# Performance work log

Hardware: AMD Instinct MI355X
Metric: run time of the kernel (lower is better)

The kernel has to match this reference:

```python
import jax, jax.numpy as jnp
import numpy as np

C = 128          # channels
N = 100000       # cells per rank (rank 0,1,2)
E_A0, E_A1, E_I1, E_I2 = 400000, 400000, 200000, 300000
NI = {"a0": 3, "a1": 6, "i1": 3, "i2": 6}   # invariant feature dims per relation
FACTOR = {"u0": 2, "u1": 3, "u2": 2}          # update-MLP concat factors


def setup_inputs() -> dict:
    key = jax.random.key(0)
    ks = iter(jax.random.split(key, 64))
    d = {}
    for name in ("f0", "f1", "f2"):
        d[name] = jax.random.normal(next(ks), (N, C), dtype=jnp.float32)
    for name, E in (("a0", E_A0), ("a1", E_A1), ("i1", E_I1), ("i2", E_I2)):
        d[name + "_send"] = jax.random.randint(next(ks), (E,), 0, N)
        d[name + "_recv"] = jax.random.randint(next(ks), (E,), 0, N)
        d["inv_" + name] = jax.random.uniform(next(ks), (E, NI[name]), dtype=jnp.float32)
        fin = 2 * C + NI[name]
        d[name + "_W1"] = jax.random.normal(next(ks), (fin, C), dtype=jnp.float32) / np.sqrt(fin)
        d[name + "_b1"] = jnp.zeros((C,), jnp.float32)
        d[name + "_W2"] = jax.random.normal(next(ks), (C, C), dtype=jnp.float32) / np.sqrt(C)
        d[name + "_b2"] = jnp.zeros((C,), jnp.float32)
        d[name + "_Wg"] = jax.random.normal(next(ks), (C, 1), dtype=jnp.float32) / np.sqrt(C)
        d[name + "_bg"] = jnp.zeros((1,), jnp.float32)
    for name, f in FACTOR.items():
        d[name + "_W1"] = jax.random.normal(next(ks), (f * C, C), dtype=jnp.float32) / np.sqrt(f * C)
        d[name + "_b1"] = jnp.zeros((C,), jnp.float32)
        d[name + "_W2"] = jax.random.normal(next(ks), (C, C), dtype=jnp.float32) / np.sqrt(C)
        d[name + "_b2"] = jnp.zeros((C,), jnp.float32)
    return d


def _econv(x_src, x_tgt, send, recv, inv, W1, b1, W2, b2, Wg, bg):
    # EConv: gather endpoints, per-edge 2-layer MLP on [x_s, x_t, invariants],
    # gated by a sigmoid edge-inference scalar (with_weighted_message=True).
    m = jnp.concatenate([x_src[send], x_tgt[recv], inv], axis=1)  # (E, 2C+ninv)
    m = jax.nn.silu(m @ W1 + b1)                                   # (E, C)
    m = jax.nn.silu(m @ W2 + b2)                                   # (E, C)
    gate = jax.nn.sigmoid(m @ Wg + bg)                             # (E, 1)
    return m * gate


def _aggregate(msg, recv, n):
    # ScatterAggregation: scatter-sum to target cells, then silu update.
    return jax.nn.silu(jax.ops.segment_sum(msg, recv, num_segments=n))


def _update(h, W1, b1, W2, b2):
    # update MLP: Linear -> SiLU -> Linear
    return jax.nn.silu(h @ W1 + b1) @ W2 + b2


def reference(f0, f1, f2,
              a0_send, a0_recv, inv_a0, a0_W1, a0_b1, a0_W2, a0_b2, a0_Wg, a0_bg,
              a1_send, a1_recv, inv_a1, a1_W1, a1_b1, a1_W2, a1_b2, a1_Wg, a1_bg,
              i1_send, i1_recv, inv_i1, i1_W1, i1_b1, i1_W2, i1_b2, i1_Wg, i1_bg,
              i2_send, i2_recv, inv_i2, i2_W1, i2_b1, i2_W2, i2_b2, i2_Wg, i2_bg,
              u0_W1, u0_b1, u0_W2, u0_b2,
              u1_W1, u1_b1, u1_W2, u1_b2,
              u2_W1, u2_b1, u2_W2, u2_b2):
    # same-rank messages (rank 0 and 1 adjacency)
    m_a0 = _aggregate(_econv(f0, f0, a0_send, a0_recv, inv_a0, a0_W1, a0_b1, a0_W2, a0_b2, a0_Wg, a0_bg), a0_recv, N)
    m_a1 = _aggregate(_econv(f1, f1, a1_send, a1_recv, inv_a1, a1_W1, a1_b1, a1_W2, a1_b2, a1_Wg, a1_bg), a1_recv, N)
    # low-to-high messages (incidence rank 0->1 and 1->2)
    m_i1 = _aggregate(_econv(f0, f1, i1_send, i1_recv, inv_i1, i1_W1, i1_b1, i1_W2, i1_b2, i1_Wg, i1_bg), i1_recv, N)
    m_i2 = _aggregate(_econv(f1, f2, i2_send, i2_recv, inv_i2, i2_W1, i2_b1, i2_W2, i2_b2, i2_Wg, i2_bg), i2_recv, N)
    # concat features with aggregated messages, update, residual add
    h0 = _update(jnp.concatenate([f0, m_a0], axis=1), u0_W1, u0_b1, u0_W2, u0_b2)
    h1 = _update(jnp.concatenate([f1, m_a1, m_i1], axis=1), u1_W1, u1_b1, u1_W2, u1_b2)
    h2 = _update(jnp.concatenate([f2, m_i2], axis=1), u2_W1, u2_b1, u2_W2, u2_b2)
    return jnp.stack([f0 + h0, f1 + h1, f2 + h2])  # (3, N, C)
```

## Files before the change

### kernel.cpp

```cpp
#include <hip/hip_runtime.h>
#include <hip/hip_bf16.h>
#include <cstdint>
#include <cstddef>

#define CDIM 128
#define NCELLS 100000

typedef __attribute__((ext_vector_type(8))) short short8;
typedef __attribute__((ext_vector_type(4))) float f32x4;

__device__ __forceinline__ unsigned short f2bf(float f) {
    unsigned u = __float_as_uint(f);
    unsigned r = u + 0x7FFFu + ((u >> 16) & 1u);
    return (unsigned short)(r >> 16);
}
__device__ __forceinline__ float bf2f(unsigned short u) {
    return __uint_as_float(((unsigned)u) << 16);
}
__device__ __forceinline__ float lo16(unsigned u) { return __uint_as_float(u << 16); }
__device__ __forceinline__ float hi16(unsigned u) { return __uint_as_float(u & 0xffff0000u); }
__device__ __forceinline__ unsigned pkbf(float lo, float hi) {
    unsigned r;
    asm("v_cvt_pk_bf16_f32 %0, %1, %2" : "=v"(r) : "v"(lo), "v"(hi));
    return r;
}
__device__ __forceinline__ unsigned short cvt1bf(float x) {
    return (unsigned short)(pkbf(x, x) & 0xffffu);
}
__device__ __forceinline__ float sigf(float x) {
    return __builtin_amdgcn_rcpf(1.f + __expf(-x));
}
__device__ __forceinline__ float siluf(float x) { return x * sigf(x); }

__device__ __forceinline__ unsigned silu2(unsigned a, unsigned b) {
    float lo = lo16(a) + lo16(b);
    float hi = hi16(a) + hi16(b);
    return pkbf(siluf(lo), siluf(hi));
}
__device__ __forceinline__ unsigned silu1(unsigned a) {
    return pkbf(siluf(lo16(a)), siluf(hi16(a)));
}

__device__ __forceinline__ void atomic_pk_bf16(void* addr, unsigned data) {
    asm volatile("global_atomic_pk_add_bf16 %0, %1, off"
                 :: "v"((unsigned long long)(uintptr_t)addr), "v"(data) : "memory");
}

__device__ __forceinline__ void load_lds16(const void* g, void* ldsbase, int lane) {
    __builtin_amdgcn_global_load_lds(
        (const __attribute__((address_space(1))) unsigned int*)(uintptr_t)g,
        (__attribute__((address_space(3))) unsigned int*)(uintptr_t)ldsbase,
        16, 0, 0);
}

struct PrepArgs {
    const float* src[14];
    int dstoff[14];
    int fin[14];
    int ktc[14];
    int tend[14];
};

__global__ void prep_kernel(PrepArgs pa, unsigned short* __restrict__ wb) {
    int tile = blockIdx.x;
    int m = 0;
    while (tile >= pa.tend[m]) m++;
    int local = tile - (m == 0 ? 0 : pa.tend[m - 1]);
    int ktc = pa.ktc[m];
    int ct = local / ktc;
    int kt = local % ktc;
    int l = threadIdx.x;
    unsigned short* dst = wb + pa.dstoff[m] + (size_t)local * 512 + l * 8;
    const float* src = pa.src[m];
    int fin = pa.fin[m];
    int col = ct * 16 + (l & 15);
#pragma unroll
    for (int i = 0; i < 8; i++) {
        int k = kt * 32 + (l >> 4) * 8 + i;
        float v = (k < fin) ? src[(size_t)k * CDIM + col] : 0.f;
        dst[i] = f2bf(v);
    }
}

__global__ void hist4_kernel(const int* __restrict__ r0, const int* __restrict__ r1,
                             const int* __restrict__ r2, const int* __restrict__ r3,
                             int E0, int E1, int E2, int E3, int* __restrict__ bins) {
    int i = blockIdx.x * blockDim.x + threadIdx.x;
    const int c1 = E0, c2 = c1 + E1, c3 = c2 + E2, c4 = c3 + E3;
    if (i >= c4) return;
    const int* r; int* b; int j;
    if (i < c1)      { r = r0; j = i;      b = bins; }
    else if (i < c2) { r = r1; j = i - c1; b = bins + (size_t)NCELLS; }
    else if (i < c3) { r = r2; j = i - c2; b = bins + (size_t)2 * NCELLS; }
    else             { r = r3; j = i - c3; b = bins + (size_t)3 * NCELLS; }
    atomicAdd(&b[r[j]], 1);
}

__global__ __launch_bounds__(1024)
void scan_kernel(const int* __restrict__ bins, int* __restrict__ offs, int NB) {
    __shared__ int wsum[16];
    __shared__ int run_s;
    const int r = blockIdx.x, t = threadIdx.x;
    const int lane = t & 63, w = t >> 6;
    const int* b = bins + (size_t)r * NB;
    int* o = offs + (size_t)r * (NB + 1);
    if (t == 0) run_s = 0;
    __syncthreads();
    for (int base = 0; base < NB; base += 1024) {
        int v = (base + t < NB) ? b[base + t] : 0;
        int x = v;
#pragma unroll
        for (int d = 1; d < 64; d <<= 1) {
            int y = __shfl_up(x, (unsigned)d, 64);
            if (lane >= d) x += y;
        }
        if (lane == 63) wsum[w] = x;
        __syncthreads();
        if (w == 0) {
            int s = (lane < 16) ? wsum[lane] : 0;
#pragma unroll
            for (int d = 1; d < 16; d <<= 1) {
                int y = __shfl_up(s, (unsigned)d, 64);
                if (lane >= d) s += y;
            }
            if (lane < 16) wsum[lane] = s;
        }
        __syncthreads();
        int woff = (w == 0) ? 0 : wsum[w - 1];
        int run = run_s;
        if (base + t < NB) o[base + t] = run + woff + x - v;
        int tot = wsum[15];
        __syncthreads();
        if (t == 0) run_s = run + tot;
        __syncthreads();
    }
    if (t == 0) o[NB] = run_s;
}

struct RankArgs {
    const int* send[4];
    const int* recv[4];
    int*  perm[4];
    int2* pair[4];
    int E[4];
    const int* offs;
    int*       cur;
};

__global__ void rank4p_kernel(RankArgs a) {
    int i = blockIdx.x * blockDim.x + threadIdx.x;
    int rel = 0, j = i;
    while (rel < 4 && j >= a.E[rel]) { j -= a.E[rel]; rel++; }
    if (rel >= 4) return;
    int v = a.recv[rel][j];
    int p = a.offs[(size_t)rel * (NCELLS + 1) + v] +
            atomicAdd(&a.cur[(size_t)rel * NCELLS + v], 1);
    a.perm[rel][p] = j;
    a.pair[rel][p] = make_int2(a.send[rel][j], v);
}

template <bool SAME>
__global__ __launch_bounds__(256, 4)
void pgemm2_kernel(const float* __restrict__ fA, const float* __restrict__ fB,
                   const unsigned short* __restrict__ W1T, const float* __restrict__ b1,
                   unsigned short* __restrict__ PA, unsigned short* __restrict__ PB,
                   int nblk)
{
    constexpr int AS = 136;
    __shared__ unsigned short A[64 * AS];

    const bool second = !SAME && ((int)blockIdx.x >= nblk);
    const float* f = second ? fB : fA;
    const int n0 = (second ? (int)blockIdx.x - nblk : (int)blockIdx.x) * 64;

    const int t = threadIdx.x;
    {
        const int rl = t >> 2, q = t & 3;
        int n = n0 + rl; n = (n < NCELLS) ? n : (NCELLS - 1);
        const float4* sp = (const float4*)(f + (size_t)n * CDIM + q * 32);
        unsigned short* arow = A + rl * AS + q * 32;
#pragma unroll
        for (int i = 0; i < 4; i++) {
            float4 a = sp[2 * i], b = sp[2 * i + 1];
            uint4 o;
            o.x = pkbf(a.x, a.y); o.y = pkbf(a.z, a.w);
            o.z = pkbf(b.x, b.y); o.w = pkbf(b.z, b.w);
            *(uint4*)(arow + i * 8) = o;
        }
    }
    __syncthreads();

    const int l = t & 63, w = t >> 6;
    const int lr = l & 15, lg = l >> 4;
    const int wr = (w & 1) * 32, wc = (w >> 1) * 64;

    const int nhalf = SAME ? 2 : 1;
#pragma unroll
    for (int h = 0; h < nhalf; h++) {
        const bool hiHalf = SAME ? (h == 1) : second;
        const int koff = hiHalf ? 4 : 0;
        unsigned short* P = hiHalf ? PB : PA;

        f32x4 acc[2][4];
#pragma unroll
        for (int mt = 0; mt < 2; mt++)
#pragma unroll
            for (int ct = 0; ct < 4; ct++) acc[mt][ct] = (f32x4){0.f, 0.f, 0.f, 0.f};

#pragma unroll
        for (int kt = 0; kt < 4; ++kt) {
            short8 av[2];
#pragma unroll
            for (int mt = 0; mt < 2; mt++)
                av[mt] = *(const short8*)(A + (wr + mt * 16 + lr) * AS + kt * 32 + lg * 8);
#pragma unroll
            for (int ct = 0; ct < 4; ct++) {
                const int cg = (wc >> 4) + ct;
                short8 bv = *(const short8*)(W1T + ((size_t)(cg * 9 + kt + koff) * 64 + l) * 8);
                acc[0][ct] = __builtin_amdgcn_mfma_f32_16x16x32_bf16(av[0], bv, acc[0][ct], 0, 0, 0);
                acc[1][ct] = __builtin_amdgcn_mfma_f32_16x16x32_bf16(av[1], bv, acc[1][ct], 0, 0, 0);
            }
        }

        float b1c[4];
#pragma unroll
        for (int ct = 0; ct < 4; ct++) b1c[ct] = hiHalf ? b1[wc + ct * 16 + lr] : 0.f;

#pragma unroll
        for (int mt = 0; mt < 2; mt++)
#pragma unroll
            for (int j = 0; j < 4; j++) {
                const int row = wr + mt * 16 + lg * 4 + j;
                const int n2  = n0 + row;
                if (n2 < NCELLS) {
#pragma unroll
                    for (int ct = 0; ct < 4; ct++)
                        P[(size_t)n2 * CDIM + wc + ct * 16 + lr] = cvt1bf(acc[mt][ct][j] + b1c[ct]);
                }
            }
    }
}

template <int NINV>
__global__ __launch_bounds__(256, 4)
void econv_kernel(const unsigned short* __restrict__ Ps, const unsigned short* __restrict__ Pt,
                  const int* __restrict__ perm, const int2* __restrict__ pair,
                  const float* __restrict__ inv,
                  const unsigned short* __restrict__ W1T,
                  const unsigned short* __restrict__ W2T, const float* __restrict__ b2,
                  const float* __restrict__ Wg, const float* __restrict__ bg,
                  unsigned short* __restrict__ acc, int E)
{
    __shared__ unsigned short PsL[64 * 128];
    __shared__ unsigned short PtL[64 * 128];
    __shared__ unsigned short Ainv[64 * 40];
    __shared__ float gpart[64];
    __shared__ int   cellid[64];

    const int t = threadIdx.x, l = t & 63, w = t >> 6;
    const int e0 = blockIdx.x * 64;

    {
        const int slot = l & 15;
        const int rsub = l >> 4;
#pragma unroll
        for (int i = 0; i < 4; i++) {
            const int r = w * 16 + i * 4 + rsub;
            int p = e0 + r; p = (p < E) ? p : (E - 1);
            const int2 sr = pair[p];
            const int ss = slot ^ (r & 7);
            load_lds16(Ps + (size_t)sr.x * CDIM + ss * 8, PsL + (w * 16 + i * 4) * 128, l);
            load_lds16(Pt + (size_t)sr.y * CDIM + ss * 8, PtL + (w * 16 + i * 4) * 128, l);
        }
    }
    if (t < 64) {
        int p = e0 + t; p = (p < E) ? p : (E - 1);
        const int j = perm[p];
        cellid[t] = pair[p].y;
        gpart[t] = 0.f;
        unsigned short* ar = Ainv + t * 40;
        const float* ip = inv + (size_t)j * NINV;
#pragma unroll
        for (int jj = 0; jj < NINV; jj++) ar[jj] = cvt1bf(ip[jj]);
#pragma unroll
        for (int jj = NINV; jj < 32; jj++) ar[jj] = 0;
    }
    __syncthreads();

    const int lr = l & 15, lg = l >> 4;
    const int wr = (w & 1) * 32;
    const int wc = (w >> 1) * 64;

    f32x4 a1[2][4];
#pragma unroll
    for (int mt = 0; mt < 2; mt++)
#pragma unroll
        for (int ct = 0; ct < 4; ct++) a1[mt][ct] = (f32x4){0.f, 0.f, 0.f, 0.f};
    {
        short8 av[2];
#pragma unroll
        for (int mt = 0; mt < 2; mt++)
            av[mt] = *(const short8*)(Ainv + (wr + mt * 16 + lr) * 40 + lg * 8);
#pragma unroll
        for (int ct = 0; ct < 4; ct++) {
            const int cg = (wc >> 4) + ct;
            short8 bv = *(const short8*)(W1T + ((size_t)(cg * 9 + 8) * 64 + l) * 8);
            a1[0][ct] = __builtin_amdgcn_mfma_f32_16x16x32_bf16(av[0], bv, a1[0][ct], 0, 0, 0);
            a1[1][ct] = __builtin_amdgcn_mfma_f32_16x16x32_bf16(av[1], bv, a1[1][ct], 0, 0, 0);
        }
    }

#pragma unroll
    for (int ct = 0; ct < 4; ct++) {
        const int col = wc + ct * 16 + lr;
#pragma unroll
        for (int mt = 0; mt < 2; mt++)
#pragma unroll
            for (int j = 0; j < 4; j++) {
                const int row = wr + mt * 16 + lg * 4 + j;
                const int idx = row * 128 + (col ^ ((row & 7) << 3));
                PtL[idx] = cvt1bf(bf2f(PtL[idx]) + a1[mt][ct][j]);
            }
    }
    __syncthreads();

    {
        const int rl = t >> 2, q = t & 3;
        unsigned short* psrow = PsL + rl * 128;
        const unsigned short* ptrow = PtL + rl * 128;
#pragma unroll
        for (int i = 0; i < 4; i++) {
            const int sl = ((q * 4 + i) ^ (rl & 7)) * 8;
            uint4 us = *(const uint4*)(psrow + sl);
            uint4 ut = *(const uint4*)(ptrow + sl);
            uint4 o;
            o.x = silu2(us.x, ut.x);
            o.y = silu2(us.y, ut.y);
            o.z = silu2(us.z, ut.z);
            o.w = silu2(us.w, ut.w);
            *(uint4*)(psrow + sl) = o;
        }
    }
    __syncthreads();

    f32x4 a2[2][4];
#pragma unroll
    for (int mt = 0; mt < 2; mt++)
#pragma unroll
        for (int ct = 0; ct < 4; ct++) a2[mt][ct] = (f32x4){0.f, 0.f, 0.f, 0.f};

#pragma unroll
    for (int kt = 0; kt < 4; ++kt) {
        short8 av[2];
#pragma unroll
        for (int mt = 0; mt < 2; mt++) {
            const int row = wr + mt * 16 + lr;
            const int sl  = (kt * 4 + lg) ^ (row & 7);
            av[mt] = *(const short8*)(PsL + row * 128 + sl * 8);
        }
#pragma unroll
        for (int ct = 0; ct < 4; ct++) {
            const int cg = (wc >> 4) + ct;
            short8 bv = *(const short8*)(W2T + ((size_t)(cg * 4 + kt) * 64 + l) * 8);
            a2[0][ct] = __builtin_amdgcn_mfma_f32_16x16x32_bf16(av[0], bv, a2[0][ct], 0, 0, 0);
            a2[1][ct] = __builtin_amdgcn_mfma_f32_16x16x32_bf16(av[1], bv, a2[1][ct], 0, 0, 0);
        }
    }

    float wg[4], b2c[4];
#pragma unroll
    for (int ct = 0; ct < 4; ct++) {
        const int col = wc + ct * 16 + lr;
        wg[ct]  = Wg[col];
        b2c[ct] = b2[col];
    }
#pragma unroll
    for (int mt = 0; mt < 2; mt++)
#pragma unroll
        for (int ct = 0; ct < 4; ct++)
#pragma unroll
            for (int j = 0; j < 4; j++)
                a2[mt][ct][j] = siluf(a2[mt][ct][j] + b2c[ct]);

#pragma unroll
    for (int mt = 0; mt < 2; mt++)
#pragma unroll
        for (int j = 0; j < 4; j++) {
            float p = a2[mt][0][j] * wg[0] + a2[mt][1][j] * wg[1] +
                      a2[mt][2][j] * wg[2] + a2[mt][3][j] * wg[3];
            p += __shfl_xor(p, 1, 16);
            p += __shfl_xor(p, 2, 16);
            p += __shfl_xor(p, 4, 16);
            p += __shfl_xor(p, 8, 16);
            if (lr == 0) atomicAdd(&gpart[wr + mt * 16 + lg * 4 + j], p);
        }
    __syncthreads();

    const float bgs = bg[0];
#pragma unroll
    for (int mt = 0; mt < 2; mt++)
#pragma unroll
        for (int j = 0; j < 4; j++) {
            const int row = wr + mt * 16 + lg * 4 + j;
            const float g = (e0 + row < E) ? sigf(gpart[row] + bgs) : 0.f;
#pragma unroll
            for (int ct = 0; ct < 4; ct++) {
                const int col = wc + ct * 16 + lr;
                PtL[row * 128 + (col ^ ((row & 7) << 3))] = cvt1bf(a2[mt][ct][j] * g);
            }
        }
    __syncthreads();

    {
        const int base = w * 16;
        int cprev, cnext;
        if (w == 0) cprev = (e0 > 0) ? pair[e0 - 1].y : -1;
        else        cprev = cellid[base - 1];
        if (w == 3) cnext = (e0 + 64 < E) ? pair[e0 + 64].y : -1;
        else        cnext = cellid[base + 16];

        unsigned vv[16];
        int cid[16];
#pragma unroll
        for (int i = 0; i < 16; i++) {
            const int r = base + i;
            const unsigned* prow = (const unsigned*)(PtL + r * 128);
            vv[i]  = prow[l ^ ((r & 7) << 2)];
            cid[i] = cellid[r];
        }

        unsigned* acc32 = (unsigned*)acc;
        float accL = 0.f, accH = 0.f;
        bool openLeft = (cid[0] == cprev);
#pragma unroll
        for (int i = 0; i < 16; i++) {
            if (i > 0 && cid[i] != cid[i - 1]) {
                const size_t di = (size_t)cid[i - 1] * 64 + l;
                if (openLeft) atomic_pk_bf16(acc32 + di, pkbf(accL, accH));
                else          acc32[di] = pkbf(accL, accH);
                accL = 0.f; accH = 0.f; openLeft = false;
            }
            accL += lo16(vv[i]);
            accH += hi16(vv[i]);
        }
        const bool openRight = (cid[15] == cnext);
        const size_t di = (size_t)cid[15] * 64 + l;
        if (openLeft || openRight) atomic_pk_bf16(acc32 + di, pkbf(accL, accH));
        else                       acc32[di] = pkbf(accL, accH);
    }
}

template <int F>
__global__ __launch_bounds__(256, F == 3 ? 3 : 4)
void update_kernel(const float* __restrict__ f,
                   const unsigned short* __restrict__ s1, const unsigned short* __restrict__ s2,
                   const unsigned short* __restrict__ W1T, const float* __restrict__ b1,
                   const unsigned short* __restrict__ W2T, const float* __restrict__ b2,
                   float* __restrict__ out)
{
    constexpr int K   = F * CDIM;
    constexpr int KT1 = K / 32;
    constexpr int AS  = K + 8;
    constexpr int YS  = 136;
    __shared__ unsigned short U[64 * AS];
    unsigned short* Alds = U;
    unsigned short* Ylds = U;

    const int t  = threadIdx.x;
    const int n0 = blockIdx.x * 64;
    const int w = t >> 6, l = t & 63;

    {
        const int rl = t >> 2, q = t & 3;
        int n = n0 + rl; n = (n < NCELLS) ? n : (NCELLS - 1);
        unsigned short* arow = Alds + rl * AS;
        {
            const float4* sp = (const float4*)(f + (size_t)n * CDIM + q * 32);
#pragma unroll
            for (int i = 0; i < 4; i++) {
                float4 a = sp[2 * i], b = sp[2 * i + 1];
                uint4 o;
                o.x = pkbf(a.x, a.y); o.y = pkbf(a.z, a.w);
                o.z = pkbf(b.x, b.y); o.w = pkbf(b.z, b.w);
                *(uint4*)(arow + q * 32 + i * 8) = o;
            }
        }
#pragma unroll
        for (int p = 1; p < F; p++) {
            const unsigned short* accp = (p == 1) ? s1 : s2;
            const uint4* sp = (const uint4*)(accp + (size_t)n * CDIM + q * 32);
            uint4* dstv = (uint4*)(arow + p * CDIM + q * 32);
#pragma unroll
            for (int i = 0; i < 4; i++) {
                uint4 v = sp[i];
                uint4 o;
                o.x = silu1(v.x); o.y = silu1(v.y);
                o.z = silu1(v.z); o.w = silu1(v.w);
                dstv[i] = o;
            }
        }
    }
    __syncthreads();

    const int lr = l & 15, lg = l >> 4;
    const int wr = (w & 1) * 32;
    const int wc = (w >> 1) * 64;

    f32x4 a1[2][4];
#pragma unroll
    for (int mt = 0; mt < 2; mt++)
#pragma unroll
        for (int ct = 0; ct < 4; ct++) a1[mt][ct] = (f32x4){0.f, 0.f, 0.f, 0.f};

    for (int kt = 0; kt < KT1; ++kt) {
        short8 av[2];
#pragma unroll
        for (int mt = 0; mt < 2; mt++)
            av[mt] = *(const short8*)(Alds + (wr + mt * 16 + lr) * AS + kt * 32 + lg * 8);
#pragma unroll
        for (int ct = 0; ct < 4; ct++) {
            const int cg = (wc >> 4) + ct;
            short8 bv = *(const short8*)(W1T + ((size_t)(cg * KT1 + kt) * 64 + l) * 8);
            a1[0][ct] = __builtin_amdgcn_mfma_f32_16x16x32_bf16(av[0], bv, a1[0][ct], 0, 0, 0);
            a1[1][ct] = __builtin_amdgcn_mfma_f32_16x16x32_bf16(av[1], bv, a1[1][ct], 0, 0, 0);
        }
    }
    __syncthreads();

#pragma unroll
    for (int ct = 0; ct < 4; ct++) {
        const int col = wc + ct * 16 + lr;
        const float bb = b1[col];
#pragma unroll
        for (int mt = 0; mt < 2; mt++)
#pragma unroll
            for (int j = 0; j < 4; j++) {
                const int row = wr + mt * 16 + lg * 4 + j;
                Ylds[row * YS + col] = cvt1bf(siluf(a1[mt][ct][j] + bb));
            }
    }
    __syncthreads();

    f32x4 a2[2][4];
#pragma unroll
    for (int mt = 0; mt < 2; mt++)
#pragma unroll
        for (int ct = 0; ct < 4; ct++) a2[mt][ct] = (f32x4){0.f, 0.f, 0.f, 0.f};

    for (int kt = 0; kt < 4; ++kt) {
        short8 av[2];
#pragma unroll
        for (int mt = 0; mt < 2; mt++)
            av[mt] = *(const short8*)(Ylds + (wr + mt * 16 + lr) * YS + kt * 32 + lg * 8);
#pragma unroll
        for (int ct = 0; ct < 4; ct++) {
            const int cg = (wc >> 4) + ct;
            short8 bv = *(const short8*)(W2T + ((size_t)(cg * 4 + kt) * 64 + l) * 8);
            a2[0][ct] = __builtin_amdgcn_mfma_f32_16x16x32_bf16(av[0], bv, a2[0][ct], 0, 0, 0);
            a2[1][ct] = __builtin_amdgcn_mfma_f32_16x16x32_bf16(av[1], bv, a2[1][ct], 0, 0, 0);
        }
    }

    float b2c[4];
#pragma unroll
    for (int ct = 0; ct < 4; ct++) b2c[ct] = b2[wc + ct * 16 + lr];

#pragma unroll
    for (int mt = 0; mt < 2; mt++)
#pragma unroll
        for (int j = 0; j < 4; j++) {
            const int row = wr + mt * 16 + lg * 4 + j;
            const int n2  = n0 + row;
            if (n2 < NCELLS) {
#pragma unroll
                for (int ct = 0; ct < 4; ct++) {
                    const int col = wc + ct * 16 + lr;
                    out[(size_t)n2 * CDIM + col] =
                        f[(size_t)n2 * CDIM + col] + a2[mt][ct][j] + b2c[ct];
                }
            }
        }
}

extern "C" void kernel_launch(void* const* d_in, const int* in_sizes, int n_in,
                              void* d_out, int out_size, void* d_ws, size_t ws_size,
                              hipStream_t stream)
{
    const float* f0 = (const float*)d_in[0];
    const float* f1 = (const float*)d_in[1];
    const float* f2 = (const float*)d_in[2];

    const int*   a0_send = (const int*)d_in[3];
    const int*   a0_recv = (const int*)d_in[4];
    const float* inv_a0  = (const float*)d_in[5];
    const float* a0_b1   = (const float*)d_in[7];
    const float* a0_b2   = (const float*)d_in[9];
    const float* a0_Wg   = (const float*)d_in[10];
    const float* a0_bg   = (const float*)d_in[11];

    const int*   a1_send = (const int*)d_in[12];
    const int*   a1_recv = (const int*)d_in[13];
    const float* inv_a1  = (const float*)d_in[14];
    const float* a1_b1   = (const float*)d_in[16];
    const float* a1_b2   = (const float*)d_in[18];
    const float* a1_Wg   = (const float*)d_in[19];
    const float* a1_bg   = (const float*)d_in[20];

    const int*   i1_send = (const int*)d_in[21];
    const int*   i1_recv = (const int*)d_in[22];
    const float* inv_i1  = (const float*)d_in[23];
    const float* i1_b1   = (const float*)d_in[25];
    const float* i1_b2   = (const float*)d_in[27];
    const float* i1_Wg   = (const float*)d_in[28];
    const float* i1_bg   = (const float*)d_in[29];

    const int*   i2_send = (const int*)d_in[30];
    const int*   i2_recv = (const int*)d_in[31];
    const float* inv_i2  = (const float*)d_in[32];
    const float* i2_b1   = (const float*)d_in[34];
    const float* i2_b2   = (const float*)d_in[36];
    const float* i2_Wg   = (const float*)d_in[37];
    const float* i2_bg   = (const float*)d_in[38];

    const float* u0_b1 = (const float*)d_in[40];
    const float* u0_b2 = (const float*)d_in[42];
    const float* u1_b1 = (const float*)d_in[44];
    const float* u1_b2 = (const float*)d_in[46];
    const float* u2_b1 = (const float*)d_in[48];
    const float* u2_b2 = (const float*)d_in[50];

    const int E_a0 = in_sizes[3];
    const int E_a1 = in_sizes[12];
    const int E_i1 = in_sizes[21];
    const int E_i2 = in_sizes[30];
    const int Es[4] = {E_a0, E_a1, E_i1, E_i2};

    char* base = (char*)d_ws;
    size_t off = 0;
    auto alloc = [&](size_t bytes) -> char* {
        off = (off + 255) & ~(size_t)255;
        char* p = base + off;
        off += bytes;
        return p;
    };
    unsigned short* wb  = (unsigned short*)alloc(753664);
    int* offs_all = (int*)alloc((size_t)4 * (NCELLS + 1) * sizeof(int));
    int* bins_all = (int*)alloc((size_t)4 * NCELLS * sizeof(int));
    int* perm[4];
    int2* pair[4];
    for (int r = 0; r < 4; r++) {
        perm[r] = (int*)alloc((size_t)Es[r] * sizeof(int));
        pair[r] = (int2*)alloc((size_t)Es[r] * sizeof(int2));
    }
    unsigned short* accA = (unsigned short*)alloc((size_t)NCELLS * CDIM * sizeof(unsigned short));
    unsigned short* accB = (unsigned short*)alloc((size_t)NCELLS * CDIM * sizeof(unsigned short));
    unsigned short* PsT = (unsigned short*)alloc((size_t)NCELLS * CDIM * sizeof(unsigned short));
    unsigned short* PtT = (unsigned short*)alloc((size_t)NCELLS * CDIM * sizeof(unsigned short));

    const int o_w1[4]  = {0, 36864, 73728, 110592};
    const int o_w2[4]  = {147456, 163840, 180224, 196608};
    const int o_uw1[3] = {212992, 245760, 294912};
    const int o_uw2[3] = {327680, 344064, 360448};

    PrepArgs pa;
    int idx = 0, cum = 0;
    auto add = [&](const void* s, int fin, int ktc, int woff) {
        pa.src[idx] = (const float*)s; pa.fin[idx] = fin; pa.ktc[idx] = ktc;
        pa.dstoff[idx] = woff; cum += ktc * 8; pa.tend[idx] = cum; idx++;
    };
    add(d_in[6],  259, 9,  o_w1[0]);
    add(d_in[15], 262, 9,  o_w1[1]);
    add(d_in[24], 259, 9,  o_w1[2]);
    add(d_in[33], 262, 9,  o_w1[3]);
    add(d_in[8],  128, 4,  o_w2[0]);
    add(d_in[17], 128, 4,  o_w2[1]);
    add(d_in[26], 128, 4,  o_w2[2]);
    add(d_in[35], 128, 4,  o_w2[3]);
    add(d_in[39], 256, 8,  o_uw1[0]);
    add(d_in[43], 384, 12, o_uw1[1]);
    add(d_in[47], 256, 8,  o_uw1[2]);
    add(d_in[41], 128, 4,  o_uw2[0]);
    add(d_in[45], 128, 4,  o_uw2[1]);
    add(d_in[49], 128, 4,  o_uw2[2]);
    prep_kernel<<<cum, 64, 0, stream>>>(pa, wb);

    const int Etot = E_a0 + E_a1 + E_i1 + E_i2;
    hipMemsetAsync(bins_all, 0, (size_t)4 * NCELLS * sizeof(int), stream);
    hist4_kernel<<<(Etot + 255) / 256, 256, 0, stream>>>(
        a0_recv, a1_recv, i1_recv, i2_recv, E_a0, E_a1, E_i1, E_i2, bins_all);
    scan_kernel<<<4, 1024, 0, stream>>>(bins_all, offs_all, NCELLS);
    hipMemsetAsync(bins_all, 0, (size_t)4 * NCELLS * sizeof(int), stream);
    {
        RankArgs ra;
        const int* sends[4] = {a0_send, a1_send, i1_send, i2_send};
        const int* recvs[4] = {a0_recv, a1_recv, i1_recv, i2_recv};
        for (int r = 0; r < 4; r++) {
            ra.send[r] = sends[r]; ra.recv[r] = recvs[r];
            ra.perm[r] = perm[r]; ra.pair[r] = pair[r]; ra.E[r] = Es[r];
        }
        ra.offs = offs_all; ra.cur = bins_all;
        rank4p_kernel<<<(Etot + 255) / 256, 256, 0, stream>>>(ra);
    }

    const size_t accBytes = (size_t)NCELLS * CDIM * sizeof(unsigned short);
    hipMemsetAsync(accA, 0, accBytes, stream);
    hipMemsetAsync(accB, 0, accBytes, stream);

    float* out = (float*)d_out;
    const int UPD_BLK = (NCELLS + 63) / 64;
    const int PG_BLK  = UPD_BLK;

    pgemm2_kernel<true><<<PG_BLK, 256, 0, stream>>>(
        f0, f0, wb + o_w1[0], a0_b1, PsT, PtT, PG_BLK);
    econv_kernel<3><<<(E_a0 + 63) / 64, 256, 0, stream>>>(
        PsT, PtT, perm[0], pair[0], inv_a0,
        wb + o_w1[0], wb + o_w2[0], a0_b2, a0_Wg, a0_bg, accA, E_a0);
    update_kernel<2><<<UPD_BLK, 256, 0, stream>>>(
        f0, accA, nullptr, wb + o_uw1[0], u0_b1, wb + o_uw2[0], u0_b2, out);
    hipMemsetAsync(accA, 0, accBytes, stream);

    pgemm2_kernel<true><<<PG_BLK, 256, 0, stream>>>(
        f1, f1, wb + o_w1[1], a1_b1, PsT, PtT, PG_BLK);
    econv_kernel<6><<<(E_a1 + 63) / 64, 256, 0, stream>>>(
        PsT, PtT, perm[1], pair[1], inv_a1,
        wb + o_w1[1], wb + o_w2[1], a1_b2, a1_Wg, a1_bg, accA, E_a1);
    pgemm2_kernel<false><<<2 * PG_BLK, 256, 0, stream>>>(
        f0, f1, wb + o_w1[2], i1_b1, PsT, PtT, PG_BLK);
    econv_kernel<3><<<(E_i1 + 63) / 64, 256, 0, stream>>>(
        PsT, PtT, perm[2], pair[2], inv_i1,
        wb + o_w1[2], wb + o_w2[2], i1_b2, i1_Wg, i1_bg, accB, E_i1);
    update_kernel<3><<<UPD_BLK, 256, 0, stream>>>(
        f1, accA, accB, wb + o_uw1[1], u1_b1, wb + o_uw2[1], u1_b2,
        out + (size_t)NCELLS * CDIM);
    hipMemsetAsync(accA, 0, accBytes, stream);

    pgemm2_kernel<false><<<2 * PG_BLK, 256, 0, stream>>>(
        f1, f2, wb + o_w1[3], i2_b1, PsT, PtT, PG_BLK);
    econv_kernel<6><<<(E_i2 + 63) / 64, 256, 0, stream>>>(
        PsT, PtT, perm[3], pair[3], inv_i2,
        wb + o_w1[3], wb + o_w2[3], i2_b2, i2_Wg, i2_bg, accA, E_i2);
    update_kernel<2><<<UPD_BLK, 256, 0, stream>>>(
        f2, accA, nullptr, wb + o_uw1[2], u2_b1, wb + o_uw2[2], u2_b2,
        out + 2 * (size_t)NCELLS * CDIM);
}
```

Baseline: 800.5 us.

## Replace serial per-relation prefix scan with three-pass chunked parallel scan

The single-block-per-relation exclusive scan over the receiver histogram is replaced by a reduce-then-scan scheme. One kernel sums 1024-bin chunks across many blocks, a small kernel scans the chunk totals, and a third kernel writes per-chunk exclusive offsets. This removes the long serial loop with repeated block barriers that ran on only four workgroups. The cost is two extra kernel launches and a small partials buffer.

```diff
diff --git a/kernel.cpp b/kernel.cpp
--- a/kernel.cpp
+++ b/kernel.cpp
@@ -5,6 +5,7 @@
 
 #define CDIM 128
 #define NCELLS 100000
+#define SCHUNK 1024
 
 typedef __attribute__((ext_vector_type(8))) short short8;
 typedef __attribute__((ext_vector_type(4))) float f32x4;
@@ -96,45 +97,76 @@
     atomicAdd(&b[r[j]], 1);
 }
 
-__global__ __launch_bounds__(1024)
-void scan_kernel(const int* __restrict__ bins, int* __restrict__ offs, int NB) {
-    __shared__ int wsum[16];
-    __shared__ int run_s;
-    const int r = blockIdx.x, t = threadIdx.x;
+__global__ void scan_sum_kernel(const int* __restrict__ bins, int* __restrict__ part,
+                                int NB, int nchunk) {
+    const int rel = blockIdx.x / nchunk;
+    const int ch  = blockIdx.x % nchunk;
+    const int t = threadIdx.x;
+    const int base = ch * SCHUNK;
+    const int* b = bins + (size_t)rel * NB + base;
+    const int lim = (NB - base < SCHUNK) ? (NB - base) : SCHUNK;
+    int s = 0;
+    for (int i = t; i < lim; i += 256) s += b[i];
+#pragma unroll
+    for (int d = 1; d < 64; d <<= 1) s += __shfl_xor(s, (unsigned)d, 64);
+    __shared__ int ws[4];
+    if ((t & 63) == 0) ws[t >> 6] = s;
+    __syncthreads();
+    if (t == 0) part[rel * nchunk + ch] = ws[0] + ws[1] + ws[2] + ws[3];
+}
+
+__global__ void scan_part_kernel(int* __restrict__ part, int* __restrict__ offs,
+                                 int NB, int nchunk) {
+    const int rel = blockIdx.x;
+    const int t = threadIdx.x;
     const int lane = t & 63, w = t >> 6;
-    const int* b = bins + (size_t)r * NB;
-    int* o = offs + (size_t)r * (NB + 1);
-    if (t == 0) run_s = 0;
-    __syncthreads();
-    for (int base = 0; base < NB; base += 1024) {
-        int v = (base + t < NB) ? b[base + t] : 0;
-        int x = v;
-#pragma unroll
-        for (int d = 1; d < 64; d <<= 1) {
-            int y = __shfl_up(x, (unsigned)d, 64);
-            if (lane >= d) x += y;
-        }
-        if (lane == 63) wsum[w] = x;
-        __syncthreads();
-        if (w == 0) {
-            int s = (lane < 16) ? wsum[lane] : 0;
-#pragma unroll
-            for (int d = 1; d < 16; d <<= 1) {
-                int y = __shfl_up(s, (unsigned)d, 64);
-                if (lane >= d) s += y;
-            }
-            if (lane < 16) wsum[lane] = s;
-        }
-        __syncthreads();
-        int woff = (w == 0) ? 0 : wsum[w - 1];
-        int run = run_s;
-        if (base + t < NB) o[base + t] = run + woff + x - v;
-        int tot = wsum[15];
-        __syncthreads();
-        if (t == 0) run_s = run + tot;
-        __syncthreads();
-    }
-    if (t == 0) o[NB] = run_s;
+    int v = (t < nchunk) ? part[rel * nchunk + t] : 0;
+    int x = v;
+#pragma unroll
+    for (int d = 1; d < 64; d <<= 1) {
+        int y = __shfl_up(x, (unsigned)d, 64);
+        if (lane >= d) x += y;
+    }
+    __shared__ int wsum[2];
+    if (lane == 63) wsum[w] = x;
+    __syncthreads();
+    if (w == 1) x += wsum[0];
+    if (t < nchunk) part[rel * nchunk + t] = x - v;
+    if (t == nchunk - 1) offs[(size_t)rel * (NB + 1) + NB] = x;
+}
+
+__global__ void scan_write_kernel(const int* __restrict__ bins, const int* __restrict__ part,
+                                  int* __restrict__ offs, int NB, int nchunk) {
+    const int rel = blockIdx.x / nchunk;
+    const int ch  = blockIdx.x % nchunk;
+    const int t = threadIdx.x;
+    const int lane = t & 63, w = t >> 6;
+    const int base = ch * SCHUNK;
+    const int* b = bins + (size_t)rel * NB + base;
+    int* o = offs + (size_t)rel * (NB + 1) + base;
+    const int lim = (NB - base < SCHUNK) ? (NB - base) : SCHUNK;
+    const int i0 = t * 4;
+    int v[4];
+#pragma unroll
+    for (int k = 0; k < 4; k++) v[k] = (i0 + k < lim) ? b[i0 + k] : 0;
+    const int tsum = v[0] + v[1] + v[2] + v[3];
+    int x = tsum;
+#pragma unroll
+    for (int d = 1; d < 64; d <<= 1) {
+        int y = __shfl_up(x, (unsigned)d, 64);
+        if (lane >= d) x += y;
+    }
+    __shared__ int wsum[4];
+    if (lane == 63) wsum[w] = x;
+    __syncthreads();
+    int woff = 0;
+#pragma unroll
+    for (int k = 0; k < 4; k++) if (k < w) woff += wsum[k];
+    int excl = woff + x - tsum + part[rel * nchunk + ch];
+#pragma unroll
+    for (int k = 0; k < 4; k++) {
+        if (i0 + k < lim) { o[i0 + k] = excl; excl += v[k]; }
+    }
 }
 
 struct RankArgs {
@@ -646,6 +678,8 @@
     unsigned short* wb  = (unsigned short*)alloc(753664);
     int* offs_all = (int*)alloc((size_t)4 * (NCELLS + 1) * sizeof(int));
     int* bins_all = (int*)alloc((size_t)4 * NCELLS * sizeof(int));
+    const int nchunk = (NCELLS + SCHUNK - 1) / SCHUNK;
+    int* part = (int*)alloc((size_t)4 * nchunk * sizeof(int));
     int* perm[4];
     int2* pair[4];
     for (int r = 0; r < 4; r++) {
@@ -688,7 +722,9 @@
     hipMemsetAsync(bins_all, 0, (size_t)4 * NCELLS * sizeof(int), stream);
     hist4_kernel<<<(Etot + 255) / 256, 256, 0, stream>>>(
         a0_recv, a1_recv, i1_recv, i2_recv, E_a0, E_a1, E_i1, E_i2, bins_all);
-    scan_kernel<<<4, 1024, 0, stream>>>(bins_all, offs_all, NCELLS);
+    scan_sum_kernel<<<4 * nchunk, 256, 0, stream>>>(bins_all, part, NCELLS, nchunk);
+    scan_part_kernel<<<4, 128, 0, stream>>>(part, offs_all, NCELLS, nchunk);
+    scan_write_kernel<<<4 * nchunk, 256, 0, stream>>>(bins_all, part, offs_all, NCELLS, nchunk);
     hipMemsetAsync(bins_all, 0, (size_t)4 * NCELLS * sizeof(int), stream);
     {
         RankArgs ra;
```

Result: faster. 720.9 us (-9.9%).
